# Kernel optimization log

Hardware: AMD Instinct MI355X
Metric: run time of the kernel (lower is better)

Reference implementation:

```python
import jax, jax.numpy as jnp
import numpy as np

N_EMBD = 384
N_HEAD = 6
HEAD_SIZE = N_EMBD // N_HEAD  # 64
B, T, S = 128, 256, 256
EPS = 1e-5


def setup_inputs() -> dict:
    key = jax.random.key(0)
    ks = jax.random.split(key, 20)
    w = lambda k, shape: (jax.random.normal(k, shape, dtype=jnp.float32) * 0.02)
    inp = {
        'x': jax.random.normal(ks[0], (B, T, N_EMBD), dtype=jnp.float32),
        'encoder_output': jax.random.normal(ks[1], (B, S, N_EMBD), dtype=jnp.float32),
        # masked self-attention heads (stacked over heads): [H, C, D]
        'wq1': w(ks[2], (N_HEAD, N_EMBD, HEAD_SIZE)),
        'wk1': w(ks[3], (N_HEAD, N_EMBD, HEAD_SIZE)),
        'wv1': w(ks[4], (N_HEAD, N_EMBD, HEAD_SIZE)),
        'proj1_w': w(ks[5], (N_EMBD, N_EMBD)),
        'proj1_b': jnp.zeros((N_EMBD,), jnp.float32),
        # cross-attention heads
        'wq2': w(ks[6], (N_HEAD, N_EMBD, HEAD_SIZE)),
        'wk2': w(ks[7], (N_HEAD, N_EMBD, HEAD_SIZE)),
        'wv2': w(ks[8], (N_HEAD, N_EMBD, HEAD_SIZE)),
        'proj2_w': w(ks[9], (N_EMBD, N_EMBD)),
        'proj2_b': jnp.zeros((N_EMBD,), jnp.float32),
        # feed-forward
        'ffn_w1': w(ks[10], (N_EMBD, 4 * N_EMBD)),
        'ffn_b1': jnp.zeros((4 * N_EMBD,), jnp.float32),
        'ffn_w2': w(ks[11], (4 * N_EMBD, N_EMBD)),
        'ffn_b2': jnp.zeros((N_EMBD,), jnp.float32),
        # layernorms
        'ln1_g': jnp.ones((N_EMBD,), jnp.float32), 'ln1_b': jnp.zeros((N_EMBD,), jnp.float32),
        'ln2_g': jnp.ones((N_EMBD,), jnp.float32), 'ln2_b': jnp.zeros((N_EMBD,), jnp.float32),
        'ln3_g': jnp.ones((N_EMBD,), jnp.float32), 'ln3_b': jnp.zeros((N_EMBD,), jnp.float32),
    }
    return inp


def _layernorm(x, g, b):
    mu = jnp.mean(x, axis=-1, keepdims=True)
    var = jnp.mean(jnp.square(x - mu), axis=-1, keepdims=True)
    return (x - mu) * jax.lax.rsqrt(var + EPS) * g + b


def _mha(xq, xkv, wq, wk, wv, proj_w, proj_b, causal):
    # NOTE: source scales by C**-0.5 with C = n_embd (not head_size)
    scale = jnp.asarray(N_EMBD, xq.dtype) ** -0.5
    q = jnp.einsum('btc,hcd->bhtd', xq, wq)
    k = jnp.einsum('bsc,hcd->bhsd', xkv, wk)
    v = jnp.einsum('bsc,hcd->bhsd', xkv, wv)
    wei = jnp.einsum('bhtd,bhsd->bhts', q, k) * scale
    if causal:
        Tq, Tk = xq.shape[1], xkv.shape[1]
        mask = jnp.tril(jnp.ones((Tq, Tk), dtype=bool))
        wei = jnp.where(mask, wei, jnp.asarray(-jnp.inf, wei.dtype))
    p = jax.nn.softmax(wei, axis=-1)  # dropout omitted (eval mode)
    o = jnp.einsum('bhts,bhsd->bhtd', p, v)
    Bq, H, Tq, D = o.shape
    o = o.transpose(0, 2, 1, 3).reshape(Bq, Tq, H * D)  # concat heads
    return o @ proj_w + proj_b


def reference(x, encoder_output,
              wq1, wk1, wv1, proj1_w, proj1_b,
              wq2, wk2, wv2, proj2_w, proj2_b,
              ffn_w1, ffn_b1, ffn_w2, ffn_b2,
              ln1_g, ln1_b, ln2_g, ln2_b, ln3_g, ln3_b):
    # x = x + masked self-attn(ln1(x))
    x = x + _mha(_layernorm(x, ln1_g, ln1_b), _layernorm(x, ln1_g, ln1_b),
                 wq1, wk1, wv1, proj1_w, proj1_b, causal=True)
    # x = x + cross-attn(ln2(x), encoder_output)  (no mask)
    x = x + _mha(_layernorm(x, ln2_g, ln2_b), encoder_output,
                 wq2, wk2, wv2, proj2_w, proj2_b, causal=False)
    # x = x + ffwd(ln3(x))
    h = _layernorm(x, ln3_g, ln3_b)
    x = x + (jax.nn.relu(h @ ffn_w1 + ffn_b1) @ ffn_w2 + ffn_b2)
    return x
```

## Files before the change

kernel.cpp:

```cpp
#include <hip/hip_runtime.h>
#include <hip/hip_bf16.h>

#define BB 128
#define TT 256
#define CC 384
#define HH 6
#define DD 64
#define NTOK 32768

typedef __attribute__((ext_vector_type(8))) short short8;
typedef __attribute__((ext_vector_type(4))) float f32x4;

__device__ __forceinline__ unsigned short f2bf(float f) {
  union { float f; unsigned int u; } v; v.f = f;
  unsigned int r = v.u + 0x7fff + ((v.u >> 16) & 1);
  return (unsigned short)(r >> 16);
}

__device__ __forceinline__ void glds16(const void* g, void* l) {
  __builtin_amdgcn_global_load_lds((const __attribute__((address_space(1))) void*)g,
                                   (__attribute__((address_space(3))) void*)l, 16, 0, 0);
}

__device__ __forceinline__ void vm_drain() {
  asm volatile("s_waitcnt vmcnt(0)" ::: "memory");
  __builtin_amdgcn_sched_barrier(0);
}

__global__ __launch_bounds__(256) void pack_t_k(
    const float* __restrict__ wq1, const float* __restrict__ wk1, const float* __restrict__ wv1,
    const float* __restrict__ wq2, const float* __restrict__ wk2, const float* __restrict__ wv2,
    const float* __restrict__ proj1_w, const float* __restrict__ proj2_w,
    const float* __restrict__ ffn_w1, const float* __restrict__ ffn_w2,
    unsigned short* __restrict__ W) {
  __shared__ unsigned short tile[64 * 72];
  const int id = blockIdx.x;
  const int tid = threadIdx.x;
  const float* src;
  unsigned short* dst;
  int ldIn, ldOut, i0, j0;
  if (id < 216) {
    int w = id / 36, rem = id - w * 36;
    int h = rem / 6, tr = rem - h * 6;
    const float* bases[6] = {wq1, wk1, wv1, wq2, wk2, wv2};
    const int dstOff[6] = {0, 147456, 294912, 442368, 589824, 737280};
    src = bases[w] + h * 24576;
    dst = W + dstOff[w] + h * 24576;
    ldIn = 64; ldOut = 384; i0 = tr * 64; j0 = 0;
  } else if (id < 288) {
    int t = id - 216;
    int which = t / 36; t -= which * 36;
    int tr = t / 6, tc = t - tr * 6;
    src = which ? proj2_w : proj1_w;
    dst = W + (which ? 1032192 : 884736);
    ldIn = 384; ldOut = 384; i0 = tr * 64; j0 = tc * 64;
  } else if (id < 432) {
    int t = id - 288;
    int tr = t / 24, tc = t - tr * 24;
    src = ffn_w1; dst = W + 1179648;
    ldIn = 1536; ldOut = 384; i0 = tr * 64; j0 = tc * 64;
  } else {
    int t = id - 432;
    int tr = t / 6, tc = t - tr * 6;
    src = ffn_w2; dst = W + 1769472;
    ldIn = 384; ldOut = 1536; i0 = tr * 64; j0 = tc * 64;
  }
#pragma unroll
  for (int p = 0; p < 4; ++p) {
    int chunk = p * 256 + tid;
    int r = chunk >> 4, c4 = chunk & 15;
    float4 f = *(const float4*)&src[(size_t)(i0 + r) * ldIn + j0 + c4 * 4];
    tile[(c4 * 4 + 0) * 72 + r] = f2bf(f.x);
    tile[(c4 * 4 + 1) * 72 + r] = f2bf(f.y);
    tile[(c4 * 4 + 2) * 72 + r] = f2bf(f.z);
    tile[(c4 * 4 + 3) * 72 + r] = f2bf(f.w);
  }
  __syncthreads();
#pragma unroll
  for (int p = 0; p < 2; ++p) {
    int chunk = p * 256 + tid;
    int j = chunk >> 3, i8 = chunk & 7;
    *(uint4*)&dst[(size_t)(j0 + j) * ldOut + i0 + i8 * 8] = *(const uint4*)&tile[j * 72 + i8 * 8];
  }
}

__global__ __launch_bounds__(256) void ln_k(const float* __restrict__ x,
                                            unsigned short* __restrict__ out,
                                            const float* __restrict__ gamma,
                                            const float* __restrict__ beta) {
  int row = blockIdx.x * 4 + (threadIdx.x >> 6);
  int lane = threadIdx.x & 63;
  const float2* xr = (const float2*)(x + (size_t)row * CC);
  float2 v[3];
  float s = 0.f;
#pragma unroll
  for (int j = 0; j < 3; ++j) { v[j] = xr[j * 64 + lane]; s += v[j].x + v[j].y; }
#pragma unroll
  for (int m = 1; m < 64; m <<= 1) s += __shfl_xor(s, m);
  float mu = s * (1.0f / CC);
  float vs = 0.f;
#pragma unroll
  for (int j = 0; j < 3; ++j) {
    float dx = v[j].x - mu, dy = v[j].y - mu;
    vs += dx * dx + dy * dy;
  }
#pragma unroll
  for (int m = 1; m < 64; m <<= 1) vs += __shfl_xor(vs, m);
  float rs = rsqrtf(vs * (1.0f / CC) + 1e-5f);
  unsigned int* orow = (unsigned int*)(out + (size_t)row * CC);
#pragma unroll
  for (int j = 0; j < 3; ++j) {
    int cidx = j * 64 + lane;
    float2 gmm = ((const float2*)gamma)[cidx];
    float2 bt = ((const float2*)beta)[cidx];
    unsigned int lo = f2bf((v[j].x - mu) * rs * gmm.x + bt.x);
    unsigned int hi = f2bf((v[j].y - mu) * rs * gmm.y + bt.y);
    orow[cidx] = lo | (hi << 16);
  }
}

template <int EPI, bool AF32, int BM>
__global__ __launch_bounds__(256) void gemm_k(const void* __restrict__ Ap, int lda,
                                              const unsigned short* __restrict__ Bt, int ldb,
                                              void* __restrict__ Cp, int ldc,
                                              const float* __restrict__ bias,
                                              const float* __restrict__ res, int ldres,
                                              int K, int nx) {
  constexpr int MI = BM / 32;
  constexpr int APASS = BM * 8 / 256;
  constexpr int LOADS = APASS + 4;
  constexpr int SMEMN = AF32 ? (BM * 64 + 8192) : 2 * (BM * 64 + 8192);
  __shared__ unsigned short smem[SMEMN];
  const int tid = threadIdx.x;
  const int chunkg = gridDim.x >> 3;
  const int wg = blockIdx.x;
  const int lg = (wg & 7) * chunkg + (wg >> 3);
  const int bx = lg % nx, by = lg / nx;
  const int m0 = by * BM;
  const int n0 = bx * 128;
  const int wid = tid >> 6, lane = tid & 63;
  const int wr = wid >> 1, wc = wid & 1;
  const int g = lane >> 4, c = lane & 15;

  f32x4 acc[MI][4] = {};
  float biasr[4];
  if (EPI >= 1) {
#pragma unroll
    for (int ni = 0; ni < 4; ++ni) biasr[ni] = bias[n0 + wc * 64 + ni * 16 + c];
  }
  const int nt = K >> 6;

  auto stageAB = [&](int t, unsigned short* sAb, unsigned short* sBb) {
    const int k0 = t * 64;
#pragma unroll
    for (int p = 0; p < APASS; ++p) {
      int chunk = p * 256 + tid;
      int row = chunk >> 3, grp = chunk & 7;
      const unsigned short* Ab = (const unsigned short*)Ap;
      glds16(&Ab[(size_t)(m0 + row) * lda + k0 + ((grp ^ (row & 7)) << 3)], &sAb[chunk * 8]);
    }
#pragma unroll
    for (int p = 0; p < 4; ++p) {
      int chunk = p * 256 + tid;
      int row = chunk >> 3, grp = chunk & 7;
      glds16(&Bt[(size_t)(n0 + row) * ldb + k0 + ((grp ^ (row & 7)) << 3)], &sBb[chunk * 8]);
    }
  };
  auto computeT = [&](const unsigned short* sAb, const unsigned short* sBb) {
#pragma unroll
    for (int kk = 0; kk < 2; ++kk) {
      short8 a[MI], b[4];
#pragma unroll
      for (int mi = 0; mi < MI; ++mi) {
        int r = wr * (BM / 2) + mi * 16 + c;
        a[mi] = *(const short8*)&sAb[r * 64 + (((kk * 4 + g) ^ (r & 7)) << 3)];
      }
#pragma unroll
      for (int ni = 0; ni < 4; ++ni) {
        int rb = wc * 64 + ni * 16 + c;
        b[ni] = *(const short8*)&sBb[rb * 64 + (((kk * 4 + g) ^ (rb & 7)) << 3)];
      }
#pragma unroll
      for (int mi = 0; mi < MI; ++mi)
#pragma unroll
        for (int ni = 0; ni < 4; ++ni)
          acc[mi][ni] = __builtin_amdgcn_mfma_f32_16x16x32_bf16(a[mi], b[ni], acc[mi][ni], 0, 0, 0);
    }
  };

  if constexpr (!AF32) {
    unsigned short* sA0 = smem;
    unsigned short* sB0 = smem + BM * 64;
    unsigned short* sA1 = smem + BM * 64 + 8192;
    unsigned short* sB1 = sA1 + BM * 64;
    stageAB(0, sA0, sB0);
    int t = 0;
    for (;;) {
      if (t + 1 < nt) {
        stageAB(t + 1, sA1, sB1);
        asm volatile("s_waitcnt vmcnt(%0)" ::"i"(LOADS) : "memory");
      } else {
        asm volatile("s_waitcnt vmcnt(0)" ::: "memory");
      }
      __builtin_amdgcn_sched_barrier(0);
      __builtin_amdgcn_s_barrier();
      computeT(sA0, sB0);
      if (t + 1 >= nt) break;
      __builtin_amdgcn_s_barrier();
      ++t;
      if (t + 1 < nt) {
        stageAB(t + 1, sA0, sB0);
        asm volatile("s_waitcnt vmcnt(%0)" ::"i"(LOADS) : "memory");
      } else {
        asm volatile("s_waitcnt vmcnt(0)" ::: "memory");
      }
      __builtin_amdgcn_sched_barrier(0);
      __builtin_amdgcn_s_barrier();
      computeT(sA1, sB1);
      if (t + 1 >= nt) break;
      __builtin_amdgcn_s_barrier();
      ++t;
    }
    __builtin_amdgcn_s_barrier();
  } else {
    unsigned short* sA = smem;
    unsigned short* sB = smem + BM * 64;
    for (int t = 0; t < nt; ++t) {
      const int k0 = t * 64;
#pragma unroll
      for (int p = 0; p < APASS; ++p) {
        int chunk = p * 256 + tid;
        int row = chunk >> 3, grp = chunk & 7;
        int dst = row * 64 + ((grp ^ (row & 7)) << 3);
        const float* Af = (const float*)Ap + (size_t)(m0 + row) * lda + k0 + grp * 8;
        float4 f0 = *(const float4*)Af;
        float4 f1 = *(const float4*)(Af + 4);
        union { unsigned short h[8]; uint4 u; } t2;
        t2.h[0] = f2bf(f0.x); t2.h[1] = f2bf(f0.y); t2.h[2] = f2bf(f0.z); t2.h[3] = f2bf(f0.w);
        t2.h[4] = f2bf(f1.x); t2.h[5] = f2bf(f1.y); t2.h[6] = f2bf(f1.z); t2.h[7] = f2bf(f1.w);
        *(uint4*)&sA[dst] = t2.u;
      }
#pragma unroll
      for (int p = 0; p < 4; ++p) {
        int chunk = p * 256 + tid;
        int row = chunk >> 3, grp = chunk & 7;
        glds16(&Bt[(size_t)(n0 + row) * ldb + k0 + ((grp ^ (row & 7)) << 3)], &sB[chunk * 8]);
      }
      vm_drain();
      __syncthreads();
      computeT(sA, sB);
      __syncthreads();
    }
  }

  if (EPI <= 1) {
#pragma unroll
    for (int mi = 0; mi < MI; ++mi)
#pragma unroll
      for (int ni = 0; ni < 4; ++ni)
#pragma unroll
        for (int i = 0; i < 4; ++i) {
          int row = wr * (BM / 2) + mi * 16 + g * 4 + i;
          int col = wc * 64 + ni * 16 + c;
          float v = acc[mi][ni][i];
          if (EPI == 1) v = fmaxf(v + biasr[ni], 0.f);
          int gsw = (col >> 3) ^ ((row >> 2) & 7);
          smem[row * 128 + gsw * 8 + (col & 7)] = f2bf(v);
        }
    __syncthreads();
#pragma unroll
    for (int it = 0; it < BM / 16; ++it) {
      int chunk = it * 256 + tid;
      int row = chunk >> 4, c16 = chunk & 15;
      int gsw = c16 ^ ((row >> 2) & 7);
      *(uint4*)&((unsigned short*)Cp)[(size_t)(m0 + row) * ldc + n0 + c16 * 8] =
          *(const uint4*)&smem[row * 128 + gsw * 8];
    }
  } else {
    float* smf = (float*)smem;
#pragma unroll
    for (int mi = 0; mi < MI; ++mi)
#pragma unroll
      for (int ni = 0; ni < 4; ++ni)
#pragma unroll
        for (int i = 0; i < 4; ++i) {
          int row = wr * (BM / 2) + mi * 16 + g * 4 + i;
          int col = wc * 64 + ni * 16 + c;
          int gg = col >> 2;
          int sg = gg ^ (row & 7);
          smf[row * 128 + sg * 4 + (col & 3)] = acc[mi][ni][i] + biasr[ni];
        }
    __syncthreads();
#pragma unroll
    for (int it = 0; it < BM / 8; ++it) {
      int chunk = it * 256 + tid;
      int row = chunk >> 5, gg = chunk & 31;
      int sg = gg ^ (row & 7);
      float4 v = *(const float4*)&smf[row * 128 + sg * 4];
      float4 r = *(const float4*)&res[(size_t)(m0 + row) * ldres + n0 + gg * 4];
      float4 o;
      o.x = v.x + r.x; o.y = v.y + r.y; o.z = v.z + r.z; o.w = v.w + r.w;
      *(float4*)&((float*)Cp)[(size_t)(m0 + row) * ldc + n0 + gg * 4] = o;
    }
  }
}

__device__ __forceinline__ int vt_off(int d, int sgrp) {
  return d * 256 + ((((sgrp + (d >> 3)) & 31) ^ (d & 7)) << 3);
}

template <bool CAUSAL>
__global__ __launch_bounds__(512, 2) void attn_k(const unsigned short* __restrict__ QKV,
                                                 unsigned short* __restrict__ O) {
  __shared__ unsigned short Ks[256 * 64];
  __shared__ unsigned short Vt[64 * 256];
  __shared__ unsigned short Ps[8][16 * 40];
  const int bh = blockIdx.x >> 1;
  const int half = blockIdx.x & 1;
  const int b = bh / HH, hh = bh - b * HH;
  const int tid = threadIdx.x, wid = tid >> 6, lane = tid & 63;
  const int g = lane >> 4, c = lane & 15;
  const unsigned short* base = QKV + (size_t)b * TT * 1152;

#pragma unroll
  for (int t = 0; t < 4; ++t) {
    int chunk = t * 512 + tid;
    int s = chunk >> 3, grp = chunk & 7;
    *(uint4*)&Ks[s * 64 + ((grp ^ (s & 7)) << 3)] =
        *(const uint4*)&base[(size_t)s * 1152 + 384 + hh * 64 + grp * 8];
    union { unsigned short h[8]; uint4 u; } tv;
    tv.u = *(const uint4*)&base[(size_t)s * 1152 + 768 + hh * 64 + grp * 8];
#pragma unroll
    for (int j = 0; j < 8; ++j) Vt[vt_off(grp * 8 + j, s >> 3) + (s & 7)] = tv.h[j];
  }
  __syncthreads();

  const float scale = 0.05103103630798287f;
  unsigned short* Pw = &Ps[wid][0];
  const int qr0 = half * 128 + wid * 16;

  short8 aq[2];
#pragma unroll
  for (int kk = 0; kk < 2; ++kk)
    aq[kk] = *(const short8*)&QKV[(size_t)(b * TT + qr0 + c) * 1152 + hh * 64 + kk * 32 + g * 8];

  f32x4 sacc[16] = {};
#pragma unroll
  for (int sj = 0; sj < 16; ++sj) {
    if (!CAUSAL || sj * 16 <= qr0) {
      int rk = sj * 16 + c;
      f32x4 z = sacc[sj];
      z = __builtin_amdgcn_mfma_f32_16x16x32_bf16(
          aq[0], *(const short8*)&Ks[rk * 64 + ((g ^ (rk & 7)) << 3)], z, 0, 0, 0);
      z = __builtin_amdgcn_mfma_f32_16x16x32_bf16(
          aq[1], *(const short8*)&Ks[rk * 64 + (((4 + g) ^ (rk & 7)) << 3)], z, 0, 0, 0);
      sacc[sj] = z;
    }
  }

  float inv[4];
#pragma unroll
  for (int i = 0; i < 4; ++i) {
    const int qr = qr0 + g * 4 + i;
    float mx = -1e30f;
#pragma unroll
    for (int sj = 0; sj < 16; ++sj) {
      if (!CAUSAL || sj * 16 <= qr0) {
        int s = sj * 16 + c;
        float v = sacc[sj][i] * scale;
        if (CAUSAL && s > qr) v = -1e30f;
        sacc[sj][i] = v;
        mx = fmaxf(mx, v);
      }
    }
#pragma unroll
    for (int m = 1; m < 16; m <<= 1) mx = fmaxf(mx, __shfl_xor(mx, m));
    float sum = 0.f;
#pragma unroll
    for (int sj = 0; sj < 16; ++sj) {
      if (!CAUSAL || sj * 16 <= qr0) {
        float p = __expf(sacc[sj][i] - mx);
        sacc[sj][i] = p;
        sum += p;
      }
    }
#pragma unroll
    for (int m = 1; m < 16; m <<= 1) sum += __shfl_xor(sum, m);
    inv[i] = 1.0f / sum;
  }

  f32x4 oacc[4] = {};
#pragma unroll
  for (int sk = 0; sk < 8; ++sk) {
    if (!CAUSAL || sk * 32 <= qr0) {
#pragma unroll
      for (int half_sj = 0; half_sj < 2; ++half_sj) {
        int sj = sk * 2 + half_sj;
#pragma unroll
        for (int i = 0; i < 4; ++i)
          Pw[(g * 4 + i) * 40 + half_sj * 16 + c] = f2bf(sacc[sj][i]);
      }
      short8 ap = *(const short8*)&Pw[c * 40 + g * 8];
#pragma unroll
      for (int dj = 0; dj < 4; ++dj) {
        short8 bv = *(const short8*)&Vt[vt_off(dj * 16 + c, sk * 4 + g)];
        oacc[dj] = __builtin_amdgcn_mfma_f32_16x16x32_bf16(ap, bv, oacc[dj], 0, 0, 0);
      }
    }
  }

  __syncthreads();
#pragma unroll
  for (int dj = 0; dj < 4; ++dj)
#pragma unroll
    for (int i = 0; i < 4; ++i) {
      int lr = wid * 16 + g * 4 + i;
      int col = dj * 16 + c;
      int gsw = (col >> 3) ^ ((lr >> 2) & 7);
      Ks[lr * 64 + gsw * 8 + (col & 7)] = f2bf(oacc[dj][i] * inv[i]);
    }
  __syncthreads();
#pragma unroll
  for (int it = 0; it < 2; ++it) {
    int chunk = it * 512 + tid;
    int row = chunk >> 3, c8 = chunk & 7;
    int gsw = c8 ^ ((row >> 2) & 7);
    *(uint4*)&O[(size_t)(b * TT + half * 128 + row) * CC + hh * 64 + c8 * 8] =
        *(const uint4*)&Ks[row * 64 + gsw * 8];
  }
}

extern "C" void kernel_launch(void* const* d_in, const int* in_sizes, int n_in,
                              void* d_out, int out_size, void* d_ws, size_t ws_size,
                              hipStream_t stream) {
  const float* x = (const float*)d_in[0];
  const float* enc = (const float*)d_in[1];
  const float* wq1 = (const float*)d_in[2];
  const float* wk1 = (const float*)d_in[3];
  const float* wv1 = (const float*)d_in[4];
  const float* proj1_w = (const float*)d_in[5];
  const float* proj1_b = (const float*)d_in[6];
  const float* wq2 = (const float*)d_in[7];
  const float* wk2 = (const float*)d_in[8];
  const float* wv2 = (const float*)d_in[9];
  const float* proj2_w = (const float*)d_in[10];
  const float* proj2_b = (const float*)d_in[11];
  const float* ffn_w1 = (const float*)d_in[12];
  const float* ffn_b1 = (const float*)d_in[13];
  const float* ffn_w2 = (const float*)d_in[14];
  const float* ffn_b2 = (const float*)d_in[15];
  const float* ln1_g = (const float*)d_in[16];
  const float* ln1_b = (const float*)d_in[17];
  const float* ln2_g = (const float*)d_in[18];
  const float* ln2_b = (const float*)d_in[19];
  const float* ln3_g = (const float*)d_in[20];
  const float* ln3_b = (const float*)d_in[21];
  float* out = (float*)d_out;

  char* ws = (char*)d_ws;
  const size_t OFF_A = 0;
  const size_t OFF_X = 50331648;
  const size_t OFF_Q = 75497472;
  const size_t OFF_O = 150994944;
  const size_t OFF_W = 176160768;

  float* xc = (float*)(ws + OFF_A);
  unsigned short* xn = (unsigned short*)(ws + OFF_X);
  unsigned short* qkv = (unsigned short*)(ws + OFF_Q);
  unsigned short* h1 = (unsigned short*)(ws + OFF_Q);
  unsigned short* obuf = (unsigned short*)(ws + OFF_O);
  unsigned short* W = (unsigned short*)(ws + OFF_W);

  unsigned short* Wqkv1t = W + 0;
  unsigned short* Wq2t = W + 442368;
  unsigned short* Wkv2t = W + 589824;
  unsigned short* proj1t = W + 884736;
  unsigned short* proj2t = W + 1032192;
  unsigned short* W1t = W + 1179648;
  unsigned short* W2t = W + 1769472;

  pack_t_k<<<576, 256, 0, stream>>>(wq1, wk1, wv1, wq2, wk2, wv2,
                                    proj1_w, proj2_w, ffn_w1, ffn_w2, W);

  dim3 blk(256);
  ln_k<<<8192, blk, 0, stream>>>(x, xn, ln1_g, ln1_b);
  gemm_k<0, false, 64><<<4608, blk, 0, stream>>>(xn, 384, Wqkv1t, 384, qkv, 1152,
                                                 nullptr, nullptr, 0, 384, 9);
  attn_k<true><<<1536, 512, 0, stream>>>(qkv, obuf);
  gemm_k<2, false, 64><<<1536, blk, 0, stream>>>(obuf, 384, proj1t, 384, xc, 384,
                                                 proj1_b, x, 384, 384, 3);
  ln_k<<<8192, blk, 0, stream>>>(xc, xn, ln2_g, ln2_b);
  gemm_k<0, false, 64><<<1536, blk, 0, stream>>>(xn, 384, Wq2t, 384, qkv, 1152,
                                                 nullptr, nullptr, 0, 384, 3);
  gemm_k<0, true, 128><<<1536, blk, 0, stream>>>(enc, 384, Wkv2t, 384, qkv + 384, 1152,
                                                 nullptr, nullptr, 0, 384, 6);
  attn_k<false><<<1536, 512, 0, stream>>>(qkv, obuf);
  gemm_k<2, false, 64><<<1536, blk, 0, stream>>>(obuf, 384, proj2t, 384, xc, 384,
                                                 proj2_b, xc, 384, 384, 3);
  ln_k<<<8192, blk, 0, stream>>>(xc, xn, ln3_g, ln3_b);
  gemm_k<1, false, 64><<<6144, blk, 0, stream>>>(xn, 384, W1t, 384, h1, 1536,
                                                 ffn_b1, nullptr, 0, 384, 12);
  gemm_k<2, false, 64><<<1536, blk, 0, stream>>>(h1, 1536, W2t, 1536, out, 384,
                                                 ffn_b2, xc, 384, 1536, 3);
}
```

Baseline: 410.8 us.

## Replace residual-add GEMMs with weight-stationary LDS kernel loading A directly to registers

Adds a bstat_k kernel for the three N=384 output projections with residual add. Each block keeps a 128x384 weight slice resident in LDS, and each of its 8 waves streams its own rows of A straight from global memory into registers, with no shared A tile. The goal is to cut repeated B tile loads and per-k-step barriers, at the cost of large LDS use (about 96KB for B alone), fewer blocks, and uncoalesced direct A loads. The generic GEMM loses its fp32 residual epilogue.

New measurement: 436.7 us. +6.3%, slower.

```diff
diff --git a/kernel.cpp b/kernel.cpp
--- a/kernel.cpp
+++ b/kernel.cpp
@@ -124,7 +124,6 @@
                                               const unsigned short* __restrict__ Bt, int ldb,
                                               void* __restrict__ Cp, int ldc,
                                               const float* __restrict__ bias,
-                                              const float* __restrict__ res, int ldres,
                                               int K, int nx) {
   constexpr int MI = BM / 32;
   constexpr int APASS = BM * 8 / 256;
@@ -253,55 +252,117 @@
     }
   }
 
-  if (EPI <= 1) {
+#pragma unroll
+  for (int mi = 0; mi < MI; ++mi)
+#pragma unroll
+    for (int ni = 0; ni < 4; ++ni)
+#pragma unroll
+      for (int i = 0; i < 4; ++i) {
+        int row = wr * (BM / 2) + mi * 16 + g * 4 + i;
+        int col = wc * 64 + ni * 16 + c;
+        float v = acc[mi][ni][i];
+        if (EPI == 1) v = fmaxf(v + biasr[ni], 0.f);
+        int gsw = (col >> 3) ^ ((row >> 2) & 7);
+        smem[row * 128 + gsw * 8 + (col & 7)] = f2bf(v);
+      }
+  __syncthreads();
+#pragma unroll
+  for (int it = 0; it < BM / 16; ++it) {
+    int chunk = it * 256 + tid;
+    int row = chunk >> 4, c16 = chunk & 15;
+    int gsw = c16 ^ ((row >> 2) & 7);
+    *(uint4*)&((unsigned short*)Cp)[(size_t)(m0 + row) * ldc + n0 + c16 * 8] =
+        *(const uint4*)&smem[row * 128 + gsw * 8];
+  }
+}
+
+template <int TR, int KCH>
+__global__ __launch_bounds__(512, 2) void bstat_k(const unsigned short* __restrict__ Ab, int lda,
+                                                  const unsigned short* __restrict__ Bt, int ldb,
+                                                  float* __restrict__ Cp, int ldc,
+                                                  const float* __restrict__ bias,
+                                                  const float* __restrict__ res, int ldres) {
+  constexpr int MI = TR / 16;
+  __shared__ unsigned short sB[128 * 384];
+  __shared__ float bounce[8][TR * 36];
+  const int tid = threadIdx.x;
+  const int chunkg = gridDim.x >> 3;
+  const int lg = (blockIdx.x & 7) * chunkg + (blockIdx.x >> 3);
+  const int p = lg % 3;
+  const int mg = lg / 3;
+  const int rowbase = mg * (8 * TR);
+  const int wid = tid >> 6, lane = tid & 63;
+  const int g = lane >> 4, c = lane & 15;
+  const int tr0 = rowbase + wid * TR;
+  const int n0 = p * 128;
+
+  f32x4 acc[MI][8] = {};
+  float biasr[8];
+#pragma unroll
+  for (int ni = 0; ni < 8; ++ni) biasr[ni] = bias[n0 + ni * 16 + c];
+
+  for (int kc = 0; kc < KCH; ++kc) {
+    if (kc) __syncthreads();
+#pragma unroll
+    for (int pp = 0; pp < 12; ++pp) {
+      int chunk = pp * 512 + tid;
+      int n = chunk / 48, k8 = chunk % 48;
+      int k8s = (k8 & ~7) | ((k8 ^ n) & 7);
+      glds16(&Bt[(size_t)(n0 + n) * ldb + kc * 384 + k8s * 8], &sB[chunk * 8]);
+    }
+    vm_drain();
+    __syncthreads();
+
+    short8 a[MI][12];
 #pragma unroll
     for (int mi = 0; mi < MI; ++mi)
 #pragma unroll
-      for (int ni = 0; ni < 4; ++ni)
+      for (int kf = 0; kf < 12; ++kf)
+        a[mi][kf] = *(const short8*)&Ab[(size_t)(tr0 + mi * 16 + c) * lda + kc * 384 +
+                                        kf * 32 + g * 8];
+#pragma unroll
+    for (int kf = 0; kf < 12; ++kf) {
+      int k8 = kf * 4 + g;
+#pragma unroll
+      for (int ni = 0; ni < 8; ++ni) {
+        int rb = ni * 16 + c;
+        int sk8 = (k8 & ~7) | ((k8 ^ rb) & 7);
+        short8 b = *(const short8*)&sB[rb * 384 + sk8 * 8];
+#pragma unroll
+        for (int mi = 0; mi < MI; ++mi)
+          acc[mi][ni] = __builtin_amdgcn_mfma_f32_16x16x32_bf16(a[mi][kf], b, acc[mi][ni], 0, 0, 0);
+      }
+    }
+  }
+
+  float* bw = bounce[wid];
+#pragma unroll
+  for (int q = 0; q < 4; ++q) {
+#pragma unroll
+    for (int mi = 0; mi < MI; ++mi)
+#pragma unroll
+      for (int nn = 0; nn < 2; ++nn) {
+        int ni = q * 2 + nn;
 #pragma unroll
         for (int i = 0; i < 4; ++i) {
-          int row = wr * (BM / 2) + mi * 16 + g * 4 + i;
-          int col = wc * 64 + ni * 16 + c;
-          float v = acc[mi][ni][i];
-          if (EPI == 1) v = fmaxf(v + biasr[ni], 0.f);
-          int gsw = (col >> 3) ^ ((row >> 2) & 7);
-          smem[row * 128 + gsw * 8 + (col & 7)] = f2bf(v);
+          int row = mi * 16 + g * 4 + i;
+          bw[row * 36 + nn * 16 + c] = acc[mi][ni][i] + biasr[ni];
         }
+      }
     __syncthreads();
 #pragma unroll
-    for (int it = 0; it < BM / 16; ++it) {
-      int chunk = it * 256 + tid;
-      int row = chunk >> 4, c16 = chunk & 15;
-      int gsw = c16 ^ ((row >> 2) & 7);
-      *(uint4*)&((unsigned short*)Cp)[(size_t)(m0 + row) * ldc + n0 + c16 * 8] =
-          *(const uint4*)&smem[row * 128 + gsw * 8];
-    }
-  } else {
-    float* smf = (float*)smem;
-#pragma unroll
-    for (int mi = 0; mi < MI; ++mi)
-#pragma unroll
-      for (int ni = 0; ni < 4; ++ni)
-#pragma unroll
-        for (int i = 0; i < 4; ++i) {
-          int row = wr * (BM / 2) + mi * 16 + g * 4 + i;
-          int col = wc * 64 + ni * 16 + c;
-          int gg = col >> 2;
-          int sg = gg ^ (row & 7);
-          smf[row * 128 + sg * 4 + (col & 3)] = acc[mi][ni][i] + biasr[ni];
-        }
-    __syncthreads();
-#pragma unroll
-    for (int it = 0; it < BM / 8; ++it) {
-      int chunk = it * 256 + tid;
-      int row = chunk >> 5, gg = chunk & 31;
-      int sg = gg ^ (row & 7);
-      float4 v = *(const float4*)&smf[row * 128 + sg * 4];
-      float4 r = *(const float4*)&res[(size_t)(m0 + row) * ldres + n0 + gg * 4];
+    for (int it = 0; it < TR / 8; ++it) {
+      int chunk = it * 64 + lane;
+      int row = chunk >> 3, gg = chunk & 7;
+      float4 v = *(const float4*)&bw[row * 36 + gg * 4];
+      int grow = tr0 + row;
+      int gcol = n0 + q * 32 + gg * 4;
+      float4 r = *(const float4*)&res[(size_t)grow * ldres + gcol];
       float4 o;
       o.x = v.x + r.x; o.y = v.y + r.y; o.z = v.z + r.z; o.w = v.w + r.w;
-      *(float4*)&((float*)Cp)[(size_t)(m0 + row) * ldc + n0 + gg * 4] = o;
-    }
+      *(float4*)&Cp[(size_t)grow * ldc + gcol] = o;
+    }
+    __syncthreads();
   }
 }
 
@@ -485,21 +546,21 @@
   dim3 blk(256);
   ln_k<<<8192, blk, 0, stream>>>(x, xn, ln1_g, ln1_b);
   gemm_k<0, false, 64><<<4608, blk, 0, stream>>>(xn, 384, Wqkv1t, 384, qkv, 1152,
-                                                 nullptr, nullptr, 0, 384, 9);
+                                                 nullptr, 384, 9);
   attn_k<true><<<1536, 512, 0, stream>>>(qkv, obuf);
-  gemm_k<2, false, 64><<<1536, blk, 0, stream>>>(obuf, 384, proj1t, 384, xc, 384,
-                                                 proj1_b, x, 384, 384, 3);
+  bstat_k<16, 1><<<768, 512, 0, stream>>>(obuf, 384, proj1t, 384, xc, 384,
+                                          proj1_b, x, 384);
   ln_k<<<8192, blk, 0, stream>>>(xc, xn, ln2_g, ln2_b);
   gemm_k<0, false, 64><<<1536, blk, 0, stream>>>(xn, 384, Wq2t, 384, qkv, 1152,
-                                                 nullptr, nullptr, 0, 384, 3);
+                                                 nullptr, 384, 3);
   gemm_k<0, true, 128><<<1536, blk, 0, stream>>>(enc, 384, Wkv2t, 384, qkv + 384, 1152,
-                                                 nullptr, nullptr, 0, 384, 6);
+                                                 nullptr, 384, 6);
   attn_k<false><<<1536, 512, 0, stream>>>(qkv, obuf);
-  gemm_k<2, false, 64><<<1536, blk, 0, stream>>>(obuf, 384, proj2t, 384, xc, 384,
-                                                 proj2_b, xc, 384, 384, 3);
+  bstat_k<16, 1><<<768, 512, 0, stream>>>(obuf, 384, proj2t, 384, xc, 384,
+                                          proj2_b, xc, 384);
   ln_k<<<8192, blk, 0, stream>>>(xc, xn, ln3_g, ln3_b);
   gemm_k<1, false, 64><<<6144, blk, 0, stream>>>(xn, 384, W1t, 384, h1, 1536,
-                                                 ffn_b1, nullptr, 0, 384, 12);
-  gemm_k<2, false, 64><<<1536, blk, 0, stream>>>(h1, 1536, W2t, 1536, out, 384,
-                                                 ffn_b2, xc, 384, 1536, 3);
-}
+                                                 ffn_b1, 384, 12);
+  bstat_k<32, 4><<<384, 512, 0, stream>>>(h1, 1536, W2t, 1536, out, 384,
+                                          ffn_b2, xc, 384);
+}
```
